# Optimization experiments

Measured on AMD Instinct MI355X. Metric: run time of the kernel, lower is better.

Reference implementation:

```python
import jax, jax.numpy as jnp
import numpy as np

ATOM_F = 64
NBR_F = 41
EPS = 1e-05


def setup_inputs() -> dict:
    key = jax.random.key(0)
    ks = jax.random.split(key, 10)
    B, N, M = 512, 64, 12
    F, NF = ATOM_F, NBR_F
    atom_fea = jax.random.normal(ks[0], (B, N, F), dtype=jnp.float32)
    nbr_fea = jax.random.normal(ks[1], (B, N, M, NF), dtype=jnp.float32)
    nbr_fea_idx = jax.random.randint(ks[2], (B, N, M), 0, N, dtype=jnp.int32)
    mask = jax.random.randint(ks[3], (B, N, M, 2 * F), 0, 2, dtype=jnp.int32)
    lim = float(np.sqrt(6.0 / (2 * F + NF + 2 * F)))
    gc_W = jax.random.uniform(ks[4], (2 * F + NF, 2 * F), minval=-lim, maxval=lim, dtype=jnp.float32)
    gc_bias = jnp.zeros((2 * F,), jnp.float32)
    gamma_1 = jnp.ones((2 * F,), jnp.float32)
    beta_1 = jnp.zeros((2 * F,), jnp.float32)
    gamma_2 = jnp.ones((F,), jnp.float32)
    beta_2 = jnp.zeros((F,), jnp.float32)
    return {
        'atom_fea': atom_fea, 'nbr_fea': nbr_fea, 'gc_W': gc_W, 'gc_bias': gc_bias,
        'gamma_1': gamma_1, 'beta_1': beta_1, 'gamma_2': gamma_2, 'beta_2': beta_2,
        'nbr_fea_idx': nbr_fea_idx, 'mask': mask,
    }


def _bn(x, mu, var, gamma, beta):
    return (x - mu) * jax.lax.rsqrt(var + EPS) * gamma + beta


def reference(atom_fea, nbr_fea, gc_W, gc_bias, gamma_1, beta_1, gamma_2, beta_2, nbr_fea_idx, mask):
    B, N, M = nbr_fea_idx.shape
    F = atom_fea.shape[-1]
    m = mask.astype(jnp.float32)                       # [B,N,M,2F]
    # gather neighbor atom features per batch: [B,N,M,F]
    atom_nbr_fea = jax.vmap(lambda af, idx: af[idx])(atom_fea, nbr_fea_idx)
    atom_exp = jnp.broadcast_to(atom_fea[:, :, None, :], (B, N, M, F))
    total_nbr_fea = jnp.concatenate([atom_exp, atom_nbr_fea, nbr_fea], axis=3)
    total_gated = (jnp.einsum('bnmk,ko->bnmo', total_nbr_fea, gc_W) + gc_bias) * m
    # global masked batchnorm (scalar mu/var over all nonzero entries)
    cnt1 = jnp.count_nonzero(total_gated).astype(jnp.float32)
    mu_1 = jnp.sum(total_gated) / cnt1
    var_1 = jnp.sum((total_gated - mu_1) ** 2 * m) / cnt1
    total_gated = _bn(total_gated, mu_1, var_1, gamma_1, beta_1) * m
    nbr_filter, nbr_core = jnp.split(total_gated, 2, axis=3)
    gated = jax.nn.sigmoid(nbr_filter) * jax.nn.softplus(nbr_core)
    m_node = m[:, :, 0, :F]                            # [B,N,F]
    nbr_summed = jnp.sum(gated, axis=2) * m_node
    cnt2 = jnp.count_nonzero(nbr_summed).astype(jnp.float32)
    mu_2 = jnp.sum(nbr_summed) / cnt2
    diff2 = (nbr_summed - mu_2) ** 2 * m_node
    var_2 = jnp.sum(diff2) / jnp.count_nonzero(diff2).astype(jnp.float32)
    nbr_summed = _bn(nbr_summed, mu_2, var_2, gamma_2, beta_2) * m_node
    return jax.nn.softplus(atom_fea + nbr_summed) * m_node
```

## Files before the change

### kernel.cpp

```cpp
#include <hip/hip_runtime.h>
#include <hip/hip_bf16.h>

#define B_   512
#define N_   64
#define M_   12
#define F_   64
#define NF_  41
#define NODES (B_*N_)
#define ROWS  (NODES*M_)
#define NPB   8
#define RPB   (NPB*M_)
#define KTOT  169
#define KPAD  192
#define ASTR  200

typedef __bf16 bf16x8 __attribute__((ext_vector_type(8)));
typedef float  f32x4  __attribute__((ext_vector_type(4)));

#define WF_OFF 128
#define X_OFF  49280

__device__ __forceinline__ float waveReduce(float v) {
#pragma unroll
  for (int off = 32; off > 0; off >>= 1) v += __shfl_down(v, off, 64);
  return v;
}

__global__ void k_wprep(const float* __restrict__ W, __bf16* __restrict__ Wf) {
  int t = blockIdx.x * 256 + threadIdx.x;
  if (t >= 6 * 8 * 64) return;
  int lane = t & 63, nt = (t >> 6) & 7, kc = t >> 9;
  int n  = nt * 16 + (lane & 15);
  int k0 = kc * 32 + (lane >> 4) * 8;
  bf16x8 v;
#pragma unroll
  for (int j = 0; j < 8; j++) {
    int k = k0 + j;
    v[j] = (k < KTOT) ? (__bf16)W[k * 128 + n] : (__bf16)0.f;
  }
  *reinterpret_cast<bf16x8*>(&Wf[(size_t)t * 8]) = v;
}

__global__ __launch_bounds__(256, 4) void k_gemm(
    const float* __restrict__ atom, const float* __restrict__ nbr,
    const int* __restrict__ idx, const int* __restrict__ mask,
    const __bf16* __restrict__ Wf, const float* __restrict__ bias,
    double* __restrict__ accum, __bf16* __restrict__ xout)
{
  __shared__ __bf16 As[RPB * ASTR];
  __shared__ int    idx_s[RPB];
  __shared__ float  red[4][4];

  const int tid = threadIdx.x;
  const int g0  = blockIdx.x * NPB;
  const int bb  = (g0 >> 6) << 6;

  if (tid < RPB) idx_s[tid] = idx[g0 * M_ + tid];
  __syncthreads();

  for (int e = tid; e < RPB * 16; e += 256) {
    int r = e >> 4, k4 = e & 15;
    int node = r / M_;
    float4 v = *(const float4*)&atom[(size_t)(g0 + node) * F_ + k4 * 4];
    __bf16 h[4] = {(__bf16)v.x, (__bf16)v.y, (__bf16)v.z, (__bf16)v.w};
    *reinterpret_cast<uint2*>(&As[r * ASTR + k4 * 4]) = *reinterpret_cast<uint2*>(h);
  }
  for (int e = tid; e < RPB * 16; e += 256) {
    int r = e >> 4, k4 = e & 15;
    float4 v = *(const float4*)&atom[(size_t)(bb + idx_s[r]) * F_ + k4 * 4];
    __bf16 h[4] = {(__bf16)v.x, (__bf16)v.y, (__bf16)v.z, (__bf16)v.w};
    *reinterpret_cast<uint2*>(&As[r * ASTR + 64 + k4 * 4]) = *reinterpret_cast<uint2*>(h);
  }
  for (int e = tid; e < RPB * NF_; e += 256) {
    int r = e / NF_, k = e - r * NF_;
    As[r * ASTR + 128 + k] = (__bf16)nbr[(size_t)(g0 * M_ + r) * NF_ + k];
  }
  for (int e = tid; e < RPB * 32; e += 256) {
    int r = e >> 5, k = 168 + (e & 31);
    if (k >= KTOT) As[r * ASTR + k] = (__bf16)0.f;
  }
  __syncthreads();

  const int w    = tid >> 6;
  const int lane = tid & 63;
  const int nlo  = lane & 15;
  const int quad = lane >> 4;

  f32x4 acc[6][2];
#pragma unroll
  for (int mt = 0; mt < 6; mt++)
#pragma unroll
    for (int j = 0; j < 2; j++) acc[mt][j] = (f32x4){0.f, 0.f, 0.f, 0.f};

#pragma unroll
  for (int kc = 0; kc < 6; kc++) {
    bf16x8 bf[2];
#pragma unroll
    for (int j = 0; j < 2; j++) {
      int nt = 2 * w + j;
      bf[j] = *reinterpret_cast<const bf16x8*>(&Wf[(size_t)(((kc * 8 + nt) * 64) + lane) * 8]);
    }
#pragma unroll
    for (int mt = 0; mt < 6; mt++) {
      bf16x8 af = *reinterpret_cast<const bf16x8*>(
          &As[(mt * 16 + nlo) * ASTR + kc * 32 + quad * 8]);
#pragma unroll
      for (int j = 0; j < 2; j++)
        acc[mt][j] = __builtin_amdgcn_mfma_f32_16x16x32_bf16(af, bf[j], acc[mt][j], 0, 0, 0);
    }
  }

  float s = 0.f, ss = 0.f, cz = 0.f, cm = 0.f;
  float bv[2];
#pragma unroll
  for (int j = 0; j < 2; j++) bv[j] = bias[(2 * w + j) * 16 + nlo];

#pragma unroll
  for (int mt = 0; mt < 6; mt++) {
#pragma unroll
    for (int reg = 0; reg < 4; reg++) {
      int rb = mt * 16 + quad * 4 + reg;
      size_t grow = (size_t)(g0 * M_) + rb;
#pragma unroll
      for (int j = 0; j < 2; j++) {
        int col = (2 * w + j) * 16 + nlo;
        int mv = mask[grow * 128 + col];
        float y = acc[mt][j][reg] + bv[j];
        y = mv ? y : 0.f;
        s += y; ss += y * y;
        cz += (y != 0.f) ? 1.f : 0.f;
        cm += (float)mv;
        xout[grow * 128 + col] = (__bf16)y;
      }
    }
  }

  float v0 = waveReduce(s), v1 = waveReduce(ss), v2 = waveReduce(cz), v3 = waveReduce(cm);
  if (lane == 0) { red[0][w] = v0; red[1][w] = v1; red[2][w] = v2; red[3][w] = v3; }
  __syncthreads();
  if (tid < 4) {
    float t = red[tid][0] + red[tid][1] + red[tid][2] + red[tid][3];
    atomicAdd(&accum[tid], (double)t);
  }
}

__global__ void k_fin1(const double* __restrict__ a, float* __restrict__ scal) {
  double s = a[0], ss = a[1], cnz = a[2], cm = a[3];
  double mu = 0.0, var = 0.0;
  if (cnz > 0.5) {
    mu = s / cnz;
    var = (ss - 2.0 * mu * s + mu * mu * cm) / cnz;
  }
  scal[0] = (float)mu;
  scal[1] = (float)(1.0 / sqrt(var + 1e-5));
}

__global__ __launch_bounds__(256) void k_act(
    const __bf16* __restrict__ x, const int* __restrict__ mask,
    const float* __restrict__ g1, const float* __restrict__ b1,
    const float* __restrict__ scal, double* __restrict__ accum,
    float* __restrict__ ns)
{
  __shared__ float red[3][4];
  int t = blockIdx.x * 256 + threadIdx.x;
  int o = t & 63;
  size_t g = (size_t)(t >> 6);
  float mu1 = scal[0], inv1 = scal[1];
  float kf = inv1 * g1[o];        float cf = b1[o]      - mu1 * kf;
  float kc = inv1 * g1[64 + o];   float cc = b1[64 + o] - mu1 * kc;
  size_t base = g * (M_ * 128) + o;
  float ssum = 0.f;
#pragma unroll
  for (int m = 0; m < M_; m++) {
    float xf = (float)x[base + m * 128];
    float xc = (float)x[base + m * 128 + 64];
    float yf = (xf != 0.f) ? fmaf(xf, kf, cf) : 0.f;
    float yc = (xc != 0.f) ? fmaf(xc, kc, cc) : 0.f;
    float sg = __builtin_amdgcn_rcpf(1.f + __expf(-yf));
    float sp = fmaxf(yc, 0.f) + __logf(1.f + __expf(-fabsf(yc)));
    ssum += sg * sp;
  }
  int mn = mask[g * (M_ * 128) + o];
  float v = mn ? ssum : 0.f;
  ns[t] = v;

  float s = v, ss = v * v, c = (v != 0.f) ? 1.f : 0.f;
  float v0 = waveReduce(s), v1 = waveReduce(ss), v2 = waveReduce(c);
  int lane = threadIdx.x & 63, wid = threadIdx.x >> 6;
  if (lane == 0) { red[0][wid] = v0; red[1][wid] = v1; red[2][wid] = v2; }
  __syncthreads();
  if (threadIdx.x < 3) {
    float r = red[threadIdx.x][0] + red[threadIdx.x][1] + red[threadIdx.x][2] + red[threadIdx.x][3];
    atomicAdd(&accum[4 + threadIdx.x], (double)r);
  }
}

__global__ void k_fin2(const double* __restrict__ a, float* __restrict__ scal) {
  double s = a[4], ss = a[5], c = a[6];
  double mu = 0.0, var = 0.0;
  if (c > 0.5) {
    mu = s / c;
    var = (ss - 2.0 * mu * s + mu * mu * c) / c;
  }
  scal[2] = (float)mu;
  scal[3] = (float)(1.0 / sqrt(var + 1e-5));
}

__global__ __launch_bounds__(256) void k_out(
    const float* __restrict__ atom, const float* __restrict__ ns,
    const float* __restrict__ g2, const float* __restrict__ b2,
    const float* __restrict__ scal, float* __restrict__ out)
{
  int t = blockIdx.x * 256 + threadIdx.x;
  int o = t & 63;
  float v = ns[t];
  float r = 0.f;
  if (v != 0.f) {
    float bn = (v - scal[2]) * scal[3] * g2[o] + b2[o];
    float a = atom[t] + bn;
    r = fmaxf(a, 0.f) + __logf(1.f + __expf(-fabsf(a)));
  }
  out[t] = r;
}

extern "C" void kernel_launch(void* const* d_in, const int* in_sizes, int n_in,
                              void* d_out, int out_size, void* d_ws, size_t ws_size,
                              hipStream_t stream)
{
  const float* atom = (const float*)d_in[0];
  const float* nbr  = (const float*)d_in[1];
  const float* W    = (const float*)d_in[2];
  const float* bias = (const float*)d_in[3];
  const float* g1   = (const float*)d_in[4];
  const float* b1   = (const float*)d_in[5];
  const float* g2   = (const float*)d_in[6];
  const float* b2   = (const float*)d_in[7];
  const int*   idx  = (const int*)d_in[8];
  const int*   mask = (const int*)d_in[9];
  float* out = (float*)d_out;

  char* ws = (char*)d_ws;
  double* accum = (double*)ws;
  float*  scal  = (float*)(ws + 64);
  __bf16* Wf    = (__bf16*)(ws + WF_OFF);
  __bf16* x     = (__bf16*)(ws + X_OFF);
  float* ns = out;

  hipMemsetAsync(d_ws, 0, 64, stream);
  k_wprep<<<12, 256, 0, stream>>>(W, Wf);
  k_gemm<<<NODES / NPB, 256, 0, stream>>>(atom, nbr, idx, mask, Wf, bias, accum, x);
  k_fin1<<<1, 1, 0, stream>>>(accum, scal);
  k_act<<<(NODES * F_) / 256, 256, 0, stream>>>(x, mask, g1, b1, scal, accum, ns);
  k_fin2<<<1, 1, 0, stream>>>(accum, scal);
  k_out<<<(NODES * F_) / 256, 256, 0, stream>>>(atom, ns, g2, b2, scal, out);
}
```

Baseline: 498.3 us.

## Stage GEMM epilogue through LDS, vectorize elementwise kernels, inline BN finalizers

The GEMM epilogue now writes its accumulators to shared memory and then reads them back row-contiguously. This allows 16-byte vectorized mask loads and bf16x8 output stores in place of scattered 2-byte stores and per-element int mask loads. The activation and output kernels process 8 features per thread with vector loads and stores. Each thread also recomputes the batchnorm mean and variance from the double accumulators, which removes the two single-thread finalize launches. The cost is an extra LDS round trip and barriers in the GEMM, plus redundant scalar double math in every thread.

```diff
diff --git a/kernel.cpp b/kernel.cpp
--- a/kernel.cpp
+++ b/kernel.cpp
@@ -11,8 +11,8 @@
 #define NPB   8
 #define RPB   (NPB*M_)
 #define KTOT  169
-#define KPAD  192
 #define ASTR  200
+#define CSTR  136
 
 typedef __bf16 bf16x8 __attribute__((ext_vector_type(8)));
 typedef float  f32x4  __attribute__((ext_vector_type(4)));
@@ -110,29 +110,43 @@
     }
   }
 
+  float bv[2];
+#pragma unroll
+  for (int j = 0; j < 2; j++) bv[j] = bias[(2 * w + j) * 16 + nlo];
+
+  __syncthreads();
+  __bf16* Cs = As;
+#pragma unroll
+  for (int mt = 0; mt < 6; mt++)
+#pragma unroll
+    for (int reg = 0; reg < 4; reg++)
+#pragma unroll
+      for (int j = 0; j < 2; j++) {
+        int row = mt * 16 + quad * 4 + reg;
+        int col = (2 * w + j) * 16 + nlo;
+        Cs[row * CSTR + col] = (__bf16)(acc[mt][j][reg] + bv[j]);
+      }
+  __syncthreads();
+
   float s = 0.f, ss = 0.f, cz = 0.f, cm = 0.f;
-  float bv[2];
-#pragma unroll
-  for (int j = 0; j < 2; j++) bv[j] = bias[(2 * w + j) * 16 + nlo];
-
-#pragma unroll
-  for (int mt = 0; mt < 6; mt++) {
-#pragma unroll
-    for (int reg = 0; reg < 4; reg++) {
-      int rb = mt * 16 + quad * 4 + reg;
-      size_t grow = (size_t)(g0 * M_) + rb;
-#pragma unroll
-      for (int j = 0; j < 2; j++) {
-        int col = (2 * w + j) * 16 + nlo;
-        int mv = mask[grow * 128 + col];
-        float y = acc[mt][j][reg] + bv[j];
-        y = mv ? y : 0.f;
-        s += y; ss += y * y;
-        cz += (y != 0.f) ? 1.f : 0.f;
-        cm += (float)mv;
-        xout[grow * 128 + col] = (__bf16)y;
-      }
-    }
+#pragma unroll
+  for (int i = 0; i < 6; i++) {
+    int ch = tid + i * 256;
+    int row = ch >> 4, c = ch & 15;
+    size_t grow = (size_t)(g0 * M_) + row;
+    bf16x8 yv = *reinterpret_cast<const bf16x8*>(&Cs[row * CSTR + c * 8]);
+    const int4 mA = *(const int4*)&mask[grow * 128 + c * 8];
+    const int4 mB = *(const int4*)&mask[grow * 128 + c * 8 + 4];
+    int mv[8] = {mA.x, mA.y, mA.z, mA.w, mB.x, mB.y, mB.z, mB.w};
+#pragma unroll
+    for (int j = 0; j < 8; j++) {
+      float y = (float)yv[j];
+      if (!mv[j]) { y = 0.f; yv[j] = (__bf16)0.f; }
+      s += y; ss += y * y;
+      cz += (y != 0.f) ? 1.f : 0.f;
+      cm += (float)mv[j];
+    }
+    *reinterpret_cast<bf16x8*>(&xout[grow * 128 + c * 8]) = yv;
   }
 
   float v0 = waveReduce(s), v1 = waveReduce(ss), v2 = waveReduce(cz), v3 = waveReduce(cm);
@@ -144,48 +158,65 @@
   }
 }
 
-__global__ void k_fin1(const double* __restrict__ a, float* __restrict__ scal) {
-  double s = a[0], ss = a[1], cnz = a[2], cm = a[3];
-  double mu = 0.0, var = 0.0;
-  if (cnz > 0.5) {
-    mu = s / cnz;
-    var = (ss - 2.0 * mu * s + mu * mu * cm) / cnz;
-  }
-  scal[0] = (float)mu;
-  scal[1] = (float)(1.0 / sqrt(var + 1e-5));
-}
-
 __global__ __launch_bounds__(256) void k_act(
     const __bf16* __restrict__ x, const int* __restrict__ mask,
     const float* __restrict__ g1, const float* __restrict__ b1,
-    const float* __restrict__ scal, double* __restrict__ accum,
-    float* __restrict__ ns)
+    double* __restrict__ accum, float* __restrict__ ns)
 {
   __shared__ float red[3][4];
   int t = blockIdx.x * 256 + threadIdx.x;
-  int o = t & 63;
-  size_t g = (size_t)(t >> 6);
-  float mu1 = scal[0], inv1 = scal[1];
-  float kf = inv1 * g1[o];        float cf = b1[o]      - mu1 * kf;
-  float kc = inv1 * g1[64 + o];   float cc = b1[64 + o] - mu1 * kc;
-  size_t base = g * (M_ * 128) + o;
-  float ssum = 0.f;
+  int g = t >> 3, o0 = (t & 7) * 8;
+
+  double S = accum[0], SS = accum[1], CNZ = accum[2], CM = accum[3];
+  float mu1 = 0.f, inv1 = 0.f;
+  if (CNZ > 0.5) {
+    double mu = S / CNZ;
+    double var = (SS - 2.0 * mu * S + mu * mu * CM) / CNZ;
+    mu1 = (float)mu; inv1 = (float)(1.0 / sqrt(var + 1e-5));
+  }
+
+  float kf[8], cf[8], kc[8], cc[8];
+#pragma unroll
+  for (int j = 0; j < 8; j++) {
+    kf[j] = inv1 * g1[o0 + j];      cf[j] = b1[o0 + j]      - mu1 * kf[j];
+    kc[j] = inv1 * g1[64 + o0 + j]; cc[j] = b1[64 + o0 + j] - mu1 * kc[j];
+  }
+
+  size_t base = (size_t)g * (M_ * 128) + o0;
+  float ssum[8];
+#pragma unroll
+  for (int j = 0; j < 8; j++) ssum[j] = 0.f;
+
 #pragma unroll
   for (int m = 0; m < M_; m++) {
-    float xf = (float)x[base + m * 128];
-    float xc = (float)x[base + m * 128 + 64];
-    float yf = (xf != 0.f) ? fmaf(xf, kf, cf) : 0.f;
-    float yc = (xc != 0.f) ? fmaf(xc, kc, cc) : 0.f;
-    float sg = __builtin_amdgcn_rcpf(1.f + __expf(-yf));
-    float sp = fmaxf(yc, 0.f) + __logf(1.f + __expf(-fabsf(yc)));
-    ssum += sg * sp;
-  }
-  int mn = mask[g * (M_ * 128) + o];
-  float v = mn ? ssum : 0.f;
-  ns[t] = v;
-
-  float s = v, ss = v * v, c = (v != 0.f) ? 1.f : 0.f;
-  float v0 = waveReduce(s), v1 = waveReduce(ss), v2 = waveReduce(c);
+    bf16x8 xf = *reinterpret_cast<const bf16x8*>(&x[base + m * 128]);
+    bf16x8 xc = *reinterpret_cast<const bf16x8*>(&x[base + m * 128 + 64]);
+#pragma unroll
+    for (int j = 0; j < 8; j++) {
+      float vf = (float)xf[j], vc = (float)xc[j];
+      float yf = (vf != 0.f) ? fmaf(vf, kf[j], cf[j]) : 0.f;
+      float yc = (vc != 0.f) ? fmaf(vc, kc[j], cc[j]) : 0.f;
+      float sg = __builtin_amdgcn_rcpf(1.f + __expf(-yf));
+      float sp = fmaxf(yc, 0.f) + __logf(1.f + __expf(-fabsf(yc)));
+      ssum[j] += sg * sp;
+    }
+  }
+
+  const int4 mA = *(const int4*)&mask[(size_t)g * (M_ * 128) + o0];
+  const int4 mB = *(const int4*)&mask[(size_t)g * (M_ * 128) + o0 + 4];
+  int mn[8] = {mA.x, mA.y, mA.z, mA.w, mB.x, mB.y, mB.z, mB.w};
+  float s = 0.f, ss2 = 0.f, c = 0.f;
+  float v[8];
+#pragma unroll
+  for (int j = 0; j < 8; j++) {
+    v[j] = mn[j] ? ssum[j] : 0.f;
+    s += v[j]; ss2 += v[j] * v[j];
+    c += (v[j] != 0.f) ? 1.f : 0.f;
+  }
+  *(float4*)&ns[(size_t)g * 64 + o0]     = (float4){v[0], v[1], v[2], v[3]};
+  *(float4*)&ns[(size_t)g * 64 + o0 + 4] = (float4){v[4], v[5], v[6], v[7]};
+
+  float v0 = waveReduce(s), v1 = waveReduce(ss2), v2 = waveReduce(c);
   int lane = threadIdx.x & 63, wid = threadIdx.x >> 6;
   if (lane == 0) { red[0][wid] = v0; red[1][wid] = v1; red[2][wid] = v2; }
   __syncthreads();
@@ -195,32 +226,40 @@
   }
 }
 
-__global__ void k_fin2(const double* __restrict__ a, float* __restrict__ scal) {
-  double s = a[4], ss = a[5], c = a[6];
-  double mu = 0.0, var = 0.0;
-  if (c > 0.5) {
-    mu = s / c;
-    var = (ss - 2.0 * mu * s + mu * mu * c) / c;
-  }
-  scal[2] = (float)mu;
-  scal[3] = (float)(1.0 / sqrt(var + 1e-5));
-}
-
 __global__ __launch_bounds__(256) void k_out(
     const float* __restrict__ atom, const float* __restrict__ ns,
     const float* __restrict__ g2, const float* __restrict__ b2,
-    const float* __restrict__ scal, float* __restrict__ out)
+    const double* __restrict__ accum, float* __restrict__ out)
 {
   int t = blockIdx.x * 256 + threadIdx.x;
-  int o = t & 63;
-  float v = ns[t];
-  float r = 0.f;
-  if (v != 0.f) {
-    float bn = (v - scal[2]) * scal[3] * g2[o] + b2[o];
-    float a = atom[t] + bn;
-    r = fmaxf(a, 0.f) + __logf(1.f + __expf(-fabsf(a)));
-  }
-  out[t] = r;
+  int g = t >> 3, o0 = (t & 7) * 8;
+
+  double S = accum[4], SS = accum[5], C = accum[6];
+  float mu2 = 0.f, inv2 = 0.f;
+  if (C > 0.5) {
+    double mu = S / C;
+    double var = (SS - 2.0 * mu * S + mu * mu * C) / C;
+    mu2 = (float)mu; inv2 = (float)(1.0 / sqrt(var + 1e-5));
+  }
+
+  float4 n0 = *(const float4*)&ns[(size_t)g * 64 + o0];
+  float4 n1 = *(const float4*)&ns[(size_t)g * 64 + o0 + 4];
+  float4 a0 = *(const float4*)&atom[(size_t)g * 64 + o0];
+  float4 a1 = *(const float4*)&atom[(size_t)g * 64 + o0 + 4];
+  float nv[8] = {n0.x, n0.y, n0.z, n0.w, n1.x, n1.y, n1.z, n1.w};
+  float av[8] = {a0.x, a0.y, a0.z, a0.w, a1.x, a1.y, a1.z, a1.w};
+  float r[8];
+#pragma unroll
+  for (int j = 0; j < 8; j++) {
+    r[j] = 0.f;
+    if (nv[j] != 0.f) {
+      float bn = (nv[j] - mu2) * inv2 * g2[o0 + j] + b2[o0 + j];
+      float a = av[j] + bn;
+      r[j] = fmaxf(a, 0.f) + __logf(1.f + __expf(-fabsf(a)));
+    }
+  }
+  *(float4*)&out[(size_t)g * 64 + o0]     = (float4){r[0], r[1], r[2], r[3]};
+  *(float4*)&out[(size_t)g * 64 + o0 + 4] = (float4){r[4], r[5], r[6], r[7]};
 }
 
 extern "C" void kernel_launch(void* const* d_in, const int* in_sizes, int n_in,
@@ -241,7 +280,6 @@
 
   char* ws = (char*)d_ws;
   double* accum = (double*)ws;
-  float*  scal  = (float*)(ws + 64);
   __bf16* Wf    = (__bf16*)(ws + WF_OFF);
   __bf16* x     = (__bf16*)(ws + X_OFF);
   float* ns = out;
@@ -249,8 +287,6 @@
   hipMemsetAsync(d_ws, 0, 64, stream);
   k_wprep<<<12, 256, 0, stream>>>(W, Wf);
   k_gemm<<<NODES / NPB, 256, 0, stream>>>(atom, nbr, idx, mask, Wf, bias, accum, x);
-  k_fin1<<<1, 1, 0, stream>>>(accum, scal);
-  k_act<<<(NODES * F_) / 256, 256, 0, stream>>>(x, mask, g1, b1, scal, accum, ns);
-  k_fin2<<<1, 1, 0, stream>>>(accum, scal);
-  k_out<<<(NODES * F_) / 256, 256, 0, stream>>>(atom, ns, g2, b2, scal, out);
-}
+  k_act<<<(NODES * 8) / 256, 256, 0, stream>>>(x, mask, g1, b1, accum, ns);
+  k_out<<<(NODES * 8) / 256, 256, 0, stream>>>(atom, ns, g2, b2, accum, out);
+}
```

After: 431.8 us. 13.3% less time.
